# Kernel tuning notes

Hardware: AMD Instinct MI355X
Metric: run time of the kernel (lower is better)

## Reference

```python
import jax, jax.numpy as jnp
import numpy as np

D_MODEL = 256
N_HEADS = 8
N_LEVELS = 4
N_POINTS = 4
SHAPES = np.array([[64, 64], [32, 32], [16, 16], [8, 8]], dtype=np.int32)


def setup_inputs() -> dict:
    key = jax.random.key(0)
    ks = jax.random.split(key, 10)
    Lq = int((SHAPES[:, 0] * SHAPES[:, 1]).sum())  # 5440
    N, d = 8, D_MODEL
    noff = N_HEADS * N_LEVELS * N_POINTS * 2
    nw = N_HEADS * N_LEVELS * N_POINTS
    s = 1.0 / np.sqrt(d).astype(np.float32)
    inp = {
        'query': jax.random.normal(ks[0], (N, Lq, d), jnp.float32),
        'reference_points': jax.random.uniform(ks[1], (N, Lq, N_LEVELS, 2), jnp.float32),
        'spatial_shapes': jnp.asarray(SHAPES),
        'level_start_index': jnp.asarray(np.concatenate([[0], np.cumsum(SHAPES[:, 0] * SHAPES[:, 1])[:-1]]).astype(np.int32)),
        'W_value': jax.random.normal(ks[2], (d, d), jnp.float32) * s,
        'b_value': jnp.zeros((d,), jnp.float32),
        'W_off': jax.random.normal(ks[3], (d, noff), jnp.float32) * 0.01,
        'b_off': jax.random.uniform(ks[4], (noff,), jnp.float32, minval=-0.5, maxval=0.5),
        'W_attn': jax.random.normal(ks[5], (d, nw), jnp.float32) * s,
        'b_attn': jnp.zeros((nw,), jnp.float32),
        'W_out': jax.random.normal(ks[6], (d, d), jnp.float32) * s,
        'b_out': jnp.zeros((d,), jnp.float32),
    }
    return inp


def _bilinear_sample(val_l, loc_l, H, W):
    # val_l: [N, h, H*W, dh] flattened level feature map
    # loc_l: [N, Lq, h, P, 2] normalized (x, y) in [0, 1]
    # grid_sample semantics, align_corners=False, zero padding
    N, h, HW, dh = val_l.shape
    Lq, P = loc_l.shape[1], loc_l.shape[3]
    x = loc_l[..., 0] * W - 0.5
    y = loc_l[..., 1] * H - 0.5
    x0 = jnp.floor(x)
    y0 = jnp.floor(y)
    wx = (x - x0)[..., None]  # [N, Lq, h, P, 1]
    wy = (y - y0)[..., None]
    x0i = x0.astype(jnp.int32)
    y0i = y0.astype(jnp.int32)

    def gather(yi, xi):
        valid = (xi >= 0) & (xi < W) & (yi >= 0) & (yi < H)  # [N, Lq, h, P]
        idx = jnp.clip(yi, 0, H - 1) * W + jnp.clip(xi, 0, W - 1)
        idx = idx.transpose(0, 2, 1, 3).reshape(N, h, Lq * P)  # [N, h, Lq*P]
        g = jnp.take_along_axis(val_l, jnp.broadcast_to(idx[..., None], (N, h, Lq * P, dh)), axis=2)
        g = g.reshape(N, h, Lq, P, dh)
        mask = valid.transpose(0, 2, 1, 3)[..., None].astype(val_l.dtype)
        return g * mask

    v00 = gather(y0i, x0i)
    v01 = gather(y0i, x0i + 1)
    v10 = gather(y0i + 1, x0i)
    v11 = gather(y0i + 1, x0i + 1)
    wxt = wx.transpose(0, 2, 1, 3, 4)  # [N, h, Lq, P, 1]
    wyt = wy.transpose(0, 2, 1, 3, 4)
    return (v00 * (1 - wxt) * (1 - wyt) + v01 * wxt * (1 - wyt)
            + v10 * (1 - wxt) * wyt + v11 * wxt * wyt)  # [N, h, Lq, P, dh]


def reference(query, reference_points, spatial_shapes, level_start_index,
              W_value, b_value, W_off, b_off, W_attn, b_attn, W_out, b_out):
    shapes = np.asarray(spatial_shapes)  # static level shapes
    N, Lq, d = query.shape
    h, L, P = N_HEADS, N_LEVELS, N_POINTS
    dh = d // h

    v = query @ W_value + b_value  # value_proj (source reassigns query = value_proj(query))
    off = (v @ W_off + b_off).reshape(N, Lq, h, L, P, 2)
    aw = jax.nn.softmax((v @ W_attn + b_attn).reshape(N, Lq, h, L * P), axis=-1)
    aw = aw.reshape(N, Lq, h, L, P)

    # offset_normalizer = [W_l, H_l]
    norm = jnp.asarray(np.stack([shapes[:, 1], shapes[:, 0]], -1), dtype=v.dtype)  # [L, 2]
    loc = reference_points[:, :, None, :, None, :] + off / norm[None, None, None, :, None, :]

    val = v.reshape(N, Lq, h, dh).transpose(0, 2, 1, 3)  # [N, h, Lv, dh]
    out = jnp.zeros((N, h, Lq, dh), v.dtype)
    start = 0
    for l in range(L):
        H, W = int(shapes[l, 0]), int(shapes[l, 1])
        val_l = val[:, :, start:start + H * W]
        sampled = _bilinear_sample(val_l, loc[:, :, :, l], H, W)  # [N, h, Lq, P, dh]
        w_l = aw[:, :, :, l].transpose(0, 2, 1, 3)[..., None]  # [N, h, Lq, P, 1]
        out = out + (sampled * w_l).sum(axis=3)
        start += H * W

    out = out.transpose(0, 2, 1, 3).reshape(N, Lq, d)
    return out @ W_out + b_out
```

## Files before the change

kernel.cpp:

```cpp
#include <hip/hip_runtime.h>
#include <hip/hip_bf16.h>
#include <cstdint>
#include <cstddef>

#define NB 8
#define LQ 5440
#define MROWS (NB * LQ)

typedef __attribute__((ext_vector_type(8))) _Float16       f16x8;
typedef __attribute__((ext_vector_type(4))) float          f32x4;
typedef __attribute__((ext_vector_type(8))) unsigned short ushort8_t;

__device__ __forceinline__ unsigned short f2h(float f) {
    _Float16 h = (_Float16)f;
    unsigned short u;
    __builtin_memcpy(&u, &h, 2);
    return u;
}
__device__ __forceinline__ float h2f(unsigned short u) {
    _Float16 h;
    __builtin_memcpy(&h, &u, 2);
    return (float)h;
}

__device__ __forceinline__ void xcd_tile(int& bx, int& by) {
    const int nx   = gridDim.x;
    const int nwg  = nx * gridDim.y;
    const int orig = blockIdx.y * nx + blockIdx.x;
    const int q = nwg >> 3, r = nwg & 7;
    const int xcd = orig & 7, pos = orig >> 3;
    const int nw = (xcd < r ? xcd * (q + 1) : r * (q + 1) + (xcd - r) * q) + pos;
    bx = nw % nx;
    by = nw / nx;
}

__global__ __launch_bounds__(256) void prep_weights(
    const float* __restrict__ Wv, const float* __restrict__ Woff,
    const float* __restrict__ Wat, const float* __restrict__ Wo,
    unsigned short* __restrict__ bigBt,
    unsigned short* __restrict__ Wv16n,
    unsigned short* __restrict__ WoaT,
    unsigned short* __restrict__ WoT)
{
    const int id = blockIdx.x * 256 + threadIdx.x;
    if (id < 65536) {
        const int n = id >> 8, k = id & 255;
        bigBt[id] = f2h(Wv[k * 256 + n]);
    } else if (id < 131072) {
        const int p = id - 65536;
        Wv16n[p] = f2h(Wv[p]);
    } else if (id < 131072 + 98304) {
        const int p = id - 131072;
        const int n = p >> 8, k = p & 255;
        WoaT[p] = (n < 256) ? f2h(Woff[k * 256 + n])
                            : f2h(Wat[k * 128 + (n - 256)]);
    } else {
        const int p = id - (131072 + 98304);
        const int n = p >> 8, k = p & 255;
        WoT[p] = f2h(Wo[k * 256 + n]);
    }
}

__global__ __launch_bounds__(256) void convert_q16(
    const float* __restrict__ q, unsigned short* __restrict__ q16)
{
    const int idx = blockIdx.x * 256 + threadIdx.x;
    const float4 a = reinterpret_cast<const float4*>(q)[idx * 2];
    const float4 b = reinterpret_cast<const float4*>(q)[idx * 2 + 1];
    ushort8_t u;
    u[0] = f2h(a.x); u[1] = f2h(a.y); u[2] = f2h(a.z); u[3] = f2h(a.w);
    u[4] = f2h(b.x); u[5] = f2h(b.y); u[6] = f2h(b.z); u[7] = f2h(b.w);
    reinterpret_cast<ushort8_t*>(q16)[idx] = u;
}

__global__ __launch_bounds__(256) void combine_bias(
    const float* __restrict__ b_value, const float* __restrict__ Woff,
    const float* __restrict__ Wat, const float* __restrict__ b_off,
    const float* __restrict__ b_attn,
    float* __restrict__ fbias, float* __restrict__ zb)
{
    const int b = blockIdx.x;
    const int t = threadIdx.x;
    if (b < 256) {
        if (t == 0) fbias[b] = b_value[b];
        return;
    }
    if (b >= 640) {
        const int i = (b - 640) * 256 + t;
        if (i < 384) zb[i] = 0.f;
        return;
    }
    const int n = b - 256;
    float p = b_value[t] * ((n < 256) ? Woff[t * 256 + n]
                                      : Wat[t * 128 + (n - 256)]);
    for (int o = 32; o >= 1; o >>= 1) p += __shfl_xor(p, o);
    __shared__ float red[4];
    if ((t & 63) == 0) red[t >> 6] = p;
    __syncthreads();
    if (t == 0) {
        float s = red[0] + red[1] + red[2] + red[3];
        fbias[b] = s + ((n < 256) ? b_off[n] : b_attn[n - 256]);
    }
}

#define BLDS 264

#define GEMM_BSTAGE_PRE()                                                     \
    __shared__ unsigned short Bs[64 * BLDS];                                  \
    int bxi, byi;                                                             \
    xcd_tile(bxi, byi);                                                       \
    const int bn = bxi * 64;                                                  \
    const int lane = threadIdx.x & 63;                                        \
    const int wid  = threadIdx.x >> 6;                                        \
    const int c    = lane & 15;                                               \
    const int qq   = lane >> 4;                                               \
    {                                                  \
        const int r  = threadIdx.x >> 2;                                      \
        const int cb = (threadIdx.x & 3) * 64;                                \
        const unsigned short* src = Bt + (size_t)(bn + r) * 256 + cb;         \
        unsigned short* dst = Bs + r * BLDS + cb;                             \
        _Pragma("unroll")                                                     \
        for (int i = 0; i < 8; ++i)                                           \
            *reinterpret_cast<ushort8_t*>(dst + i * 8) =                      \
                *reinterpret_cast<const ushort8_t*>(src + i * 8);             \
    }                                                                         \
    __syncthreads();

#define GEMM_PANEL_CORE(bm)                                                   \
    const int wr = (bm) + wid * 32;                                           \
    const unsigned short* pa0 = At + (size_t)(wr + c) * 256 + qq * 8;         \
    const unsigned short* pa1 = pa0 + 16 * 256;                               \
    f32x4 acc[2][4];                                                          \
    _Pragma("unroll")                                                         \
    for (int s = 0; s < 2; ++s)                                               \
        _Pragma("unroll")                                                     \
        for (int j = 0; j < 4; ++j)                                           \
            acc[s][j] = (f32x4){0.f, 0.f, 0.f, 0.f};                          \
    _Pragma("unroll")                                                         \
    for (int ks = 0; ks < 8; ++ks) {                                          \
        const int o = ks * 32;                                                \
        const f16x8 a0 = *reinterpret_cast<const f16x8*>(pa0 + o);            \
        const f16x8 a1 = *reinterpret_cast<const f16x8*>(pa1 + o);            \
        f16x8 bf[4];                                                          \
        _Pragma("unroll")                                                     \
        for (int j = 0; j < 4; ++j)                                           \
            bf[j] = *reinterpret_cast<const f16x8*>(                          \
                Bs + (j * 16 + c) * BLDS + o + qq * 8);                       \
        _Pragma("unroll")                                                     \
        for (int j = 0; j < 4; ++j) {                                         \
            acc[0][j] = __builtin_amdgcn_mfma_f32_16x16x32_f16(               \
                a0, bf[j], acc[0][j], 0, 0, 0);                               \
            acc[1][j] = __builtin_amdgcn_mfma_f32_16x16x32_f16(               \
                a1, bf[j], acc[1][j], 0, 0, 0);                               \
        }                                                                     \
    }

template<int PANELS, bool F16_OUT>
__global__ __launch_bounds__(256) void gemm_bstage(
    const unsigned short* __restrict__ At, const unsigned short* __restrict__ Bt,
    const float* __restrict__ bias0, const float* __restrict__ bias1,
    void* __restrict__ C0, void* __restrict__ C1,
    int cs0, int cs1, int split)
{
    GEMM_BSTAGE_PRE();

#pragma unroll
    for (int p = 0; p < PANELS; ++p) {
        GEMM_PANEL_CORE((byi * PANELS + p) * 128);

#pragma unroll
        for (int j = 0; j < 4; ++j) {
            const int col    = bn + j * 16 + c;
            const bool second = col >= split;
            const int ccol   = second ? col - split : col;
            const float bv   = second ? bias1[ccol] : bias0[ccol];
#pragma unroll
            for (int s = 0; s < 2; ++s) {
#pragma unroll
                for (int r = 0; r < 4; ++r) {
                    const int row = wr + s * 16 + qq * 4 + r;
                    const float v0 = acc[s][j][r] + bv;
                    if (F16_OUT) {
                        const float v1 = __shfl_xor(v0, 1);
                        if ((lane & 1) == 0) {
                            const unsigned int packed =
                                (unsigned int)f2h(v0) | ((unsigned int)f2h(v1) << 16);
                            unsigned short* Cb = (unsigned short*)(second ? C1 : C0);
                            const int cs = second ? cs1 : cs0;
                            *reinterpret_cast<unsigned int*>(
                                Cb + (size_t)row * cs + ccol) = packed;
                        }
                    } else {
                        float* Cf = (float*)C0;
                        Cf[(size_t)row * cs0 + col] = v0;
                    }
                }
            }
        }
    }
}

template<int PANELS>
__global__ __launch_bounds__(256) void gemm_front(
    const unsigned short* __restrict__ At, const unsigned short* __restrict__ Bt,
    const float* __restrict__ fbias,
    unsigned short* __restrict__ v16, unsigned short* __restrict__ off16,
    unsigned short* __restrict__ at16)
{
    GEMM_BSTAGE_PRE();

#pragma unroll
    for (int p = 0; p < PANELS; ++p) {
        GEMM_PANEL_CORE((byi * PANELS + p) * 128);

#pragma unroll
        for (int j = 0; j < 4; ++j) {
            const int col  = bn + j * 16 + c;
            const float bv = fbias[col];
#pragma unroll
            for (int s = 0; s < 2; ++s) {
#pragma unroll
                for (int r = 0; r < 4; ++r) {
                    const int row = wr + s * 16 + qq * 4 + r;
                    const float v0 = acc[s][j][r] + bv;
                    const float v1 = __shfl_xor(v0, 1);
                    if ((lane & 1) == 0) {
                        const unsigned int packed =
                            (unsigned int)f2h(v0) | ((unsigned int)f2h(v1) << 16);
                        unsigned short* dst;
                        if (col < 256)      dst = v16   + (size_t)row * 256 + col;
                        else if (col < 512) dst = off16 + (size_t)row * 256 + (col - 256);
                        else                dst = at16  + (size_t)row * 128 + (col - 512);
                        *reinterpret_cast<unsigned int*>(dst) = packed;
                    }
                }
            }
        }
    }
}

__global__ __launch_bounds__(256) void sample_kernel(
    const unsigned short* __restrict__ v16,
    const unsigned short* __restrict__ off16,
    const unsigned short* __restrict__ attn16,
    const float* __restrict__ refpts,
    unsigned short* __restrict__ pre16)
{
    const int lane = threadIdx.x & 63;
    const int wv   = threadIdx.x >> 6;
    const int bid  = (blockIdx.x & 7) * 1360 + (blockIdx.x >> 3);
    const int row  = bid * 4 + wv;
    const int n    = row / LQ;

    __shared__ uint4 swi[4][328];

    const ushort4 o4 = reinterpret_cast<const ushort4*>(off16)[(size_t)row * 64 + lane];
    const unsigned int lg = reinterpret_cast<const unsigned int*>(attn16)[(size_t)row * 64 + lane];
    const float l0 = h2f((unsigned short)(lg & 0xffff));
    const float l1 = h2f((unsigned short)(lg >> 16));

    const int h   = lane >> 3;
    const int k   = lane & 7;
    const int lev = k >> 1;
    const float rx = refpts[(size_t)row * 8 + lev * 2 + 0];
    const float ry = refpts[(size_t)row * 8 + lev * 2 + 1];

    float m = fmaxf(l0, l1);
    m = fmaxf(m, __shfl_xor(m, 1));
    m = fmaxf(m, __shfl_xor(m, 2));
    m = fmaxf(m, __shfl_xor(m, 4));
    const float e0 = __expf(l0 - m);
    const float e1 = __expf(l1 - m);
    float s = e0 + e1;
    s += __shfl_xor(s, 1);
    s += __shfl_xor(s, 2);
    s += __shfl_xor(s, 4);
    const float inv = 1.f / s;

    const int  W     = 64 >> lev;
    const int  start = (lev == 0) ? 0 : (lev == 1) ? 4096 : (lev == 2) ? 5120 : 5376;
    const float rs   = 0.015625f * (float)(1 << lev);

#pragma unroll
    for (int pp = 0; pp < 2; ++pp) {
        const float lx = rx + h2f(pp ? o4.z : o4.x) * rs;
        const float ly = ry + h2f(pp ? o4.w : o4.y) * rs;
        const float wgt = (pp ? e1 : e0) * inv;

        const float x = lx * (float)W - 0.5f;
        const float y = ly * (float)W - 0.5f;
        const float fx = floorf(x), fy = floorf(y);
        const int xi = (int)fx, yi = (int)fy;
        const float wx = x - fx, wy = y - fy;

        const int x0 = min(max(xi, 0), W - 1);
        const int x1 = min(max(xi + 1, 0), W - 1);
        const int y0 = min(max(yi, 0), W - 1);
        const int y1 = min(max(yi + 1, 0), W - 1);
        const float vx0 = (xi >= 0 && xi < W)         ? (1.f - wx) : 0.f;
        const float vx1 = (xi + 1 >= 0 && xi + 1 < W) ? wx         : 0.f;
        const float vy0 = (yi >= 0 && yi < W)         ? (1.f - wy) : 0.f;
        const float vy1 = (yi + 1 >= 0 && yi + 1 < W) ? wy         : 0.f;

        const int hb  = h * 64;
        const unsigned int b00 = (unsigned int)((start + y0 * W + x0) * 512 + hb);
        const unsigned int b01 = (unsigned int)((start + y0 * W + x1) * 512 + hb);
        const unsigned int b10 = (unsigned int)((start + y1 * W + x0) * 512 + hb);
        const unsigned int b11 = (unsigned int)((start + y1 * W + x1) * 512 + hb);

        uint4 c0, c1;
        c0.x = __float_as_uint(wgt * vy0 * vx0);
        c0.y = __float_as_uint(wgt * vy0 * vx1);
        c0.z = b00; c0.w = b01;
        c1.x = __float_as_uint(wgt * vy1 * vx0);
        c1.y = __float_as_uint(wgt * vy1 * vx1);
        c1.z = b10; c1.w = b11;
        const int base = h * 41 + 5 * k + 2 * pp;
        swi[wv][base + 0] = c0;
        swi[wv][base + 1] = c1;
    }
    __syncthreads();

    const int cp = (lane >> 2) & 1;
    const int cg = lane & 3;
    const unsigned int koff = cg * 16;

    const int nu = __builtin_amdgcn_readfirstlane(n);
    const char* vn = reinterpret_cast<const char*>(v16) + (size_t)nu * (LQ * 512);
    const uint4* wib = &swi[wv][h * 41 + cp];

#define OFS(j) (2 * (j) + ((j) >> 1))
#define GLD(o) (*reinterpret_cast<const ushort8_t*>(vn + ((o) + koff)))

    float acc[8];
#pragma unroll
    for (int i = 0; i < 8; ++i) acc[i] = 0.f;

    uint4 wi0 = wib[OFS(0)];
    uint4 wi1 = wib[OFS(1)];
    uint4 wi2 = wib[OFS(2)];
    uint4 wi3 = wi2;
    ushort8_t va0 = GLD(wi0.z), vb0 = GLD(wi0.w);
    ushort8_t va1 = GLD(wi1.z), vb1 = GLD(wi1.w);
    ushort8_t va2 = va1,        vb2 = vb1;

#pragma unroll
    for (int j = 0; j < 16; ++j) {
        if (j <= 13) { va2 = GLD(wi2.z); vb2 = GLD(wi2.w); }
        if (j <= 12) wi3 = wib[OFS(j + 3)];

        const float wa = __uint_as_float(wi0.x);
        const float wb = __uint_as_float(wi0.y);
#pragma unroll
        for (int i = 0; i < 8; ++i)
            acc[i] = fmaf(h2f(va0[i]), wa, acc[i]);
#pragma unroll
        for (int i = 0; i < 8; ++i)
            acc[i] = fmaf(h2f(vb0[i]), wb, acc[i]);

        wi0 = wi1; wi1 = wi2; wi2 = wi3;
        va0 = va1; va1 = va2; vb0 = vb1; vb1 = vb2;
    }
#undef OFS
#undef GLD

#pragma unroll
    for (int i = 0; i < 8; ++i)
        acc[i] += __shfl_xor(acc[i], 4);

    if (cp == 0) {
        ushort8_t st;
#pragma unroll
        for (int i = 0; i < 8; ++i) st[i] = f2h(acc[i]);
        *reinterpret_cast<ushort8_t*>(
            pre16 + (size_t)row * 256 + h * 32 + cg * 8) = st;
    }
}

extern "C" void kernel_launch(void* const* d_in, const int* in_sizes, int n_in,
                              void* d_out, int out_size, void* d_ws, size_t ws_size,
                              hipStream_t stream)
{
    const float* query   = (const float*)d_in[0];
    const float* refpts  = (const float*)d_in[1];
    const float* W_value = (const float*)d_in[4];
    const float* b_value = (const float*)d_in[5];
    const float* W_off   = (const float*)d_in[6];
    const float* b_off   = (const float*)d_in[7];
    const float* W_attn  = (const float*)d_in[8];
    const float* b_attn  = (const float*)d_in[9];
    const float* W_out   = (const float*)d_in[10];
    const float* b_out   = (const float*)d_in[11];
    float* out = (float*)d_out;

    unsigned short* ws_v16   = (unsigned short*)d_ws;
    unsigned short* ws_off16 = ws_v16   + (size_t)MROWS * 256;
    unsigned short* ws_at16  = ws_off16 + (size_t)MROWS * 256;
    unsigned short* ws_pre16 = ws_at16  + (size_t)MROWS * 128;
    unsigned short* ws_q16   = ws_pre16 + (size_t)MROWS * 256;
    unsigned short* ws_bigBt = ws_q16   + (size_t)MROWS * 256;
    unsigned short* ws_wv16n = ws_bigBt + 640 * 256;
    unsigned short* ws_woaT  = ws_wv16n + 65536;
    unsigned short* ws_woT   = ws_woaT  + 98304;
    float*          ws_fbias = (float*)(ws_woT + 65536);
    float*          ws_zb    = ws_fbias + 640;

    prep_weights<<<dim3(1152), 256, 0, stream>>>(
        W_value, W_off, W_attn, W_out, ws_bigBt, ws_wv16n, ws_woaT, ws_woT);

    combine_bias<<<dim3(642), 256, 0, stream>>>(
        b_value, W_off, W_attn, b_off, b_attn, ws_fbias, ws_zb);

    convert_q16<<<dim3(5440), 256, 0, stream>>>(query, ws_q16);

    gemm_bstage<1, true><<<dim3(4, 3), 256, 0, stream>>>(
        ws_woaT, ws_wv16n, ws_zb, ws_zb,
        ws_bigBt + 65536, ws_bigBt + 65536, 256, 256, 1 << 30);

    gemm_front<2><<<dim3(10, 170), 256, 0, stream>>>(
        ws_q16, ws_bigBt, ws_fbias, ws_v16, ws_off16, ws_at16);

    sample_kernel<<<dim3(MROWS / 4), 256, 0, stream>>>(
        ws_v16, ws_off16, ws_at16, refpts, ws_pre16);

    gemm_bstage<2, false><<<dim3(4, 170), 256, 0, stream>>>(
        ws_pre16, ws_woT, b_out, b_out, out, out, 256, 256, 1 << 30);
}
```

Measured before the change: 145.1 us.

## Prefetch next A panel into registers and raise panels per block to five

The GEMM kernels now load the whole A panel for the next 128-row slab into a register double-buffer while MFMAs run on the current one. The per-block panel count rises from 2 to 5, which cuts the grid from 170 to 68 row-blocks and amortizes the staged B tile over more rows. Per-column output routing and bias selection are hoisted out of the inner store loops. The cost is much higher register pressure (two 2x8 f16x8 buffers per lane), which may reduce occupancy, and a smaller grid that may underfill the CUs.

```diff
diff --git a/kernel.cpp b/kernel.cpp
--- a/kernel.cpp
+++ b/kernel.cpp
@@ -105,7 +105,7 @@
 
 #define BLDS 264
 
-#define GEMM_BSTAGE_PRE()                                                     \
+#define GEMM_B_PRE()                                                          \
     __shared__ unsigned short Bs[64 * BLDS];                                  \
     int bxi, byi;                                                             \
     xcd_tile(bxi, byi);                                                       \
@@ -126,11 +126,19 @@
     }                                                                         \
     __syncthreads();
 
-#define GEMM_PANEL_CORE(bm)                                                   \
-    const int wr = (bm) + wid * 32;                                           \
-    const unsigned short* pa0 = At + (size_t)(wr + c) * 256 + qq * 8;         \
-    const unsigned short* pa1 = pa0 + 16 * 256;                               \
-    f32x4 acc[2][4];                                                          \
+#define PANEL_A_LOAD(buf, prow)                                               \
+    {                                                                         \
+        const unsigned short* pa =                                            \
+            At + (size_t)((prow) + c) * 256 + qq * 8;                         \
+        _Pragma("unroll")                                                     \
+        for (int ks = 0; ks < 8; ++ks) {                                      \
+            Ar[buf][0][ks] = *reinterpret_cast<const f16x8*>(pa + ks * 32);   \
+            Ar[buf][1][ks] = *reinterpret_cast<const f16x8*>(                 \
+                pa + 16 * 256 + ks * 32);                                     \
+        }                                                                     \
+    }
+
+#define PANEL_COMPUTE(buf)                                                    \
     _Pragma("unroll")                                                         \
     for (int s = 0; s < 2; ++s)                                               \
         _Pragma("unroll")                                                     \
@@ -138,63 +146,79 @@
             acc[s][j] = (f32x4){0.f, 0.f, 0.f, 0.f};                          \
     _Pragma("unroll")                                                         \
     for (int ks = 0; ks < 8; ++ks) {                                          \
-        const int o = ks * 32;                                                \
-        const f16x8 a0 = *reinterpret_cast<const f16x8*>(pa0 + o);            \
-        const f16x8 a1 = *reinterpret_cast<const f16x8*>(pa1 + o);            \
         f16x8 bf[4];                                                          \
         _Pragma("unroll")                                                     \
         for (int j = 0; j < 4; ++j)                                           \
             bf[j] = *reinterpret_cast<const f16x8*>(                          \
-                Bs + (j * 16 + c) * BLDS + o + qq * 8);                       \
+                Bs + (j * 16 + c) * BLDS + ks * 32 + qq * 8);                 \
         _Pragma("unroll")                                                     \
         for (int j = 0; j < 4; ++j) {                                         \
             acc[0][j] = __builtin_amdgcn_mfma_f32_16x16x32_f16(               \
-                a0, bf[j], acc[0][j], 0, 0, 0);                               \
+                Ar[buf][0][ks], bf[j], acc[0][j], 0, 0, 0);                   \
             acc[1][j] = __builtin_amdgcn_mfma_f32_16x16x32_f16(               \
-                a1, bf[j], acc[1][j], 0, 0, 0);                               \
+                Ar[buf][1][ks], bf[j], acc[1][j], 0, 0, 0);                   \
         }                                                                     \
     }
 
 template<int PANELS, bool F16_OUT>
-__global__ __launch_bounds__(256) void gemm_bstage(
+__global__ __launch_bounds__(256) void gemm_panels(
     const unsigned short* __restrict__ At, const unsigned short* __restrict__ Bt,
     const float* __restrict__ bias0, const float* __restrict__ bias1,
     void* __restrict__ C0, void* __restrict__ C1,
     int cs0, int cs1, int split)
 {
-    GEMM_BSTAGE_PRE();
+    GEMM_B_PRE();
+
+    const bool second = (bn >= split);
+    const int cs2 = second ? cs1 : cs0;
+    const int cb  = second ? bn - split : bn;
+    const float* bp = second ? bias1 : bias0;
+
+    f16x8 Ar[2][2][8];
+    f32x4 acc[2][4];
+
+    PANEL_A_LOAD(0, (byi * PANELS) * 128 + wid * 32);
 
 #pragma unroll
     for (int p = 0; p < PANELS; ++p) {
-        GEMM_PANEL_CORE((byi * PANELS + p) * 128);
-
-#pragma unroll
-        for (int j = 0; j < 4; ++j) {
-            const int col    = bn + j * 16 + c;
-            const bool second = col >= split;
-            const int ccol   = second ? col - split : col;
-            const float bv   = second ? bias1[ccol] : bias0[ccol];
-#pragma unroll
-            for (int s = 0; s < 2; ++s) {
-#pragma unroll
-                for (int r = 0; r < 4; ++r) {
-                    const int row = wr + s * 16 + qq * 4 + r;
-                    const float v0 = acc[s][j][r] + bv;
-                    if (F16_OUT) {
+        if (p + 1 < PANELS)
+            PANEL_A_LOAD((p + 1) & 1, (byi * PANELS + p + 1) * 128 + wid * 32);
+
+        PANEL_COMPUTE(p & 1);
+
+        const int wr = (byi * PANELS + p) * 128 + wid * 32;
+        if (F16_OUT) {
+            unsigned short* dstB = (unsigned short*)(second ? C1 : C0);
+#pragma unroll
+            for (int j = 0; j < 4; ++j) {
+                const float bv = bp[cb + j * 16 + c];
+#pragma unroll
+                for (int s = 0; s < 2; ++s)
+#pragma unroll
+                    for (int r = 0; r < 4; ++r) {
+                        const float v0 = acc[s][j][r] + bv;
                         const float v1 = __shfl_xor(v0, 1);
                         if ((lane & 1) == 0) {
-                            const unsigned int packed =
-                                (unsigned int)f2h(v0) | ((unsigned int)f2h(v1) << 16);
-                            unsigned short* Cb = (unsigned short*)(second ? C1 : C0);
-                            const int cs = second ? cs1 : cs0;
-                            *reinterpret_cast<unsigned int*>(
-                                Cb + (size_t)row * cs + ccol) = packed;
+                            const unsigned packed =
+                                (unsigned)f2h(v0) | ((unsigned)f2h(v1) << 16);
+                            const int row = wr + s * 16 + qq * 4 + r;
+                            *reinterpret_cast<unsigned*>(
+                                dstB + (size_t)row * cs2 + cb + j * 16 + c) = packed;
                         }
-                    } else {
-                        float* Cf = (float*)C0;
-                        Cf[(size_t)row * cs0 + col] = v0;
                     }
-                }
+            }
+        } else {
+            float* Cf = (float*)C0;
+#pragma unroll
+            for (int j = 0; j < 4; ++j) {
+                const float bv = bias0[bn + j * 16 + c];
+#pragma unroll
+                for (int s = 0; s < 2; ++s)
+#pragma unroll
+                    for (int r = 0; r < 4; ++r) {
+                        const int row = wr + s * 16 + qq * 4 + r;
+                        Cf[(size_t)row * cs0 + bn + j * 16 + c] = acc[s][j][r] + bv;
+                    }
             }
         }
     }
@@ -207,34 +231,44 @@
     unsigned short* __restrict__ v16, unsigned short* __restrict__ off16,
     unsigned short* __restrict__ at16)
 {
-    GEMM_BSTAGE_PRE();
+    GEMM_B_PRE();
+
+    unsigned short* dstB;
+    int cs2, cb;
+    if (bn < 256)      { dstB = v16;   cs2 = 256; cb = bn; }
+    else if (bn < 512) { dstB = off16; cs2 = 256; cb = bn - 256; }
+    else               { dstB = at16;  cs2 = 128; cb = bn - 512; }
+
+    f16x8 Ar[2][2][8];
+    f32x4 acc[2][4];
+
+    PANEL_A_LOAD(0, (byi * PANELS) * 128 + wid * 32);
 
 #pragma unroll
     for (int p = 0; p < PANELS; ++p) {
-        GEMM_PANEL_CORE((byi * PANELS + p) * 128);
-
+        if (p + 1 < PANELS)
+            PANEL_A_LOAD((p + 1) & 1, (byi * PANELS + p + 1) * 128 + wid * 32);
+
+        PANEL_COMPUTE(p & 1);
+
+        const int wr = (byi * PANELS + p) * 128 + wid * 32;
 #pragma unroll
         for (int j = 0; j < 4; ++j) {
-            const int col  = bn + j * 16 + c;
-            const float bv = fbias[col];
-#pragma unroll
-            for (int s = 0; s < 2; ++s) {
+            const float bv = fbias[bn + j * 16 + c];
+#pragma unroll
+            for (int s = 0; s < 2; ++s)
 #pragma unroll
                 for (int r = 0; r < 4; ++r) {
-                    const int row = wr + s * 16 + qq * 4 + r;
                     const float v0 = acc[s][j][r] + bv;
                     const float v1 = __shfl_xor(v0, 1);
                     if ((lane & 1) == 0) {
-                        const unsigned int packed =
-                            (unsigned int)f2h(v0) | ((unsigned int)f2h(v1) << 16);
-                        unsigned short* dst;
-                        if (col < 256)      dst = v16   + (size_t)row * 256 + col;
-                        else if (col < 512) dst = off16 + (size_t)row * 256 + (col - 256);
-                        else                dst = at16  + (size_t)row * 128 + (col - 512);
-                        *reinterpret_cast<unsigned int*>(dst) = packed;
+                        const unsigned packed =
+                            (unsigned)f2h(v0) | ((unsigned)f2h(v1) << 16);
+                        const int row = wr + s * 16 + qq * 4 + r;
+                        *reinterpret_cast<unsigned*>(
+                            dstB + (size_t)row * cs2 + cb + j * 16 + c) = packed;
                     }
                 }
-            }
         }
     }
 }
@@ -413,16 +447,16 @@
 
     convert_q16<<<dim3(5440), 256, 0, stream>>>(query, ws_q16);
 
-    gemm_bstage<1, true><<<dim3(4, 3), 256, 0, stream>>>(
+    gemm_panels<1, true><<<dim3(4, 3), 256, 0, stream>>>(
         ws_woaT, ws_wv16n, ws_zb, ws_zb,
         ws_bigBt + 65536, ws_bigBt + 65536, 256, 256, 1 << 30);
 
-    gemm_front<2><<<dim3(10, 170), 256, 0, stream>>>(
+    gemm_front<5><<<dim3(10, 68), 256, 0, stream>>>(
         ws_q16, ws_bigBt, ws_fbias, ws_v16, ws_off16, ws_at16);
 
     sample_kernel<<<dim3(MROWS / 4), 256, 0, stream>>>(
         ws_v16, ws_off16, ws_at16, refpts, ws_pre16);
 
-    gemm_bstage<2, false><<<dim3(4, 170), 256, 0, stream>>>(
+    gemm_panels<5, false><<<dim3(4, 68), 256, 0, stream>>>(
         ws_pre16, ws_woT, b_out, b_out, out, out, 256, 256, 1 << 30);
 }
```

New measurement: 158.1 us. +9.0%, slower.
